# Performance work log

Measured on AMD Instinct MI355X. Metric: run time of the kernel, lower is better.

## Reference

```python
import jax, jax.numpy as jnp
import numpy as np

D_MODEL = 1024
N_HEADS = 16
D_K = D_MODEL // N_HEADS
SEQ = 4096
BATCH = 2
THETA = 10000.0


def _rope(x, token_positions):
    # x: [b, h, s, d_k], token_positions: [s] int
    half = D_K // 2
    inv_freq = 1.0 / (THETA ** (jnp.arange(0, D_K, 2, dtype=jnp.float32) / D_K))  # [half]
    freqs = token_positions.astype(jnp.float32)[:, None] * inv_freq[None, :]      # [s, half]
    cos, sin = jnp.cos(freqs), jnp.sin(freqs)                                     # [s, half]
    xe = x[..., 0::2]
    xo = x[..., 1::2]
    out_e = xe * cos - xo * sin
    out_o = xe * sin + xo * cos
    # interleave even/odd back: [..., s, half, 2] -> [..., s, d_k]
    return jnp.stack([out_e, out_o], axis=-1).reshape(x.shape)


def setup_inputs() -> dict:
    key = jax.random.key(0)
    ks = jax.random.split(key, 5)
    std = (2.0 / (D_MODEL + D_MODEL)) ** 0.5
    x = jax.random.normal(ks[0], (BATCH, SEQ, D_MODEL), dtype=jnp.float32)
    Wq = jax.random.normal(ks[1], (D_MODEL, D_MODEL), dtype=jnp.float32) * std
    Wk = jax.random.normal(ks[2], (D_MODEL, D_MODEL), dtype=jnp.float32) * std
    Wv = jax.random.normal(ks[3], (D_MODEL, D_MODEL), dtype=jnp.float32) * std
    Wo = jax.random.normal(ks[4], (D_MODEL, D_MODEL), dtype=jnp.float32) * std
    token_positions = jnp.arange(SEQ, dtype=jnp.int32)
    return {"x": x, "token_positions": token_positions, "Wq": Wq, "Wk": Wk, "Wv": Wv, "Wo": Wo}


def reference(x, token_positions, Wq, Wk, Wv, Wo):
    B, S, _ = x.shape

    def proj(W):
        y = jnp.einsum('bsd,od->bso', x, W)                     # [b, s, d_model]
        return y.reshape(B, S, N_HEADS, D_K).transpose(0, 2, 1, 3)  # [b, h, s, d_k]

    q, k, v = proj(Wq), proj(Wk), proj(Wv)
    q = _rope(q, token_positions)
    k = _rope(k, token_positions)

    scale = 1.0 / np.sqrt(D_K).astype(np.float32)
    scores = jnp.einsum('bhqd,bhkd->bhqk', q, k) * scale        # [b, h, s, s]
    causal = jnp.tril(jnp.ones((S, S), dtype=bool))
    scores = jnp.where(causal[None, None], scores, -jnp.inf)
    probs = jax.nn.softmax(scores, axis=-1)
    out = jnp.einsum('bhqk,bhkd->bhqd', probs, v)               # [b, h, s, d_k]
    out = out.transpose(0, 2, 1, 3).reshape(B, S, D_MODEL)
    return jnp.einsum('bsd,od->bso', out, Wo)
```

## Files before the change

kernel.cpp:

```cpp
#include <hip/hip_runtime.h>
#include <hip/hip_bf16.h>

typedef unsigned short u16;
typedef __attribute__((ext_vector_type(4))) float f32x4;
typedef __attribute__((ext_vector_type(16))) float f32x16;
typedef __attribute__((ext_vector_type(8))) short s16x8;
typedef __attribute__((ext_vector_type(2))) unsigned u32x2;

constexpr int DMODEL = 1024;
constexpr int NH     = 16;
constexpr int DK     = 64;
constexpr int SEQ    = 4096;
constexpr int BATCH  = 2;
constexpr int BS     = BATCH * SEQ;
constexpr int NX     = BS * DMODEL;
constexpr int NW     = DMODEL * DMODEL;
constexpr float QSC  = 0.18033688011112042f;

__device__ __forceinline__ unsigned pk2(float a, float b) {
  float2 t; t.x = a; t.y = b;
  __hip_bfloat162 h = __float22bfloat162_rn(t);
  return *reinterpret_cast<unsigned*>(&h);
}
__device__ __forceinline__ u32x2 plswap(unsigned a, unsigned b) {
  return __builtin_amdgcn_permlane32_swap(a, b, false, false);
}
__device__ __forceinline__ f32x16 mfma32(s16x8 a, s16x8 b, f32x16 c) {
  return __builtin_amdgcn_mfma_f32_32x32x16_bf16(a, b, c, 0, 0, 0);
}
__device__ __forceinline__ void gload_lds16(const void* g, void* l) {
  __builtin_amdgcn_global_load_lds(
      (const __attribute__((address_space(1))) void*)g,
      (__attribute__((address_space(3))) void*)l, 16, 0, 0);
}
__device__ __forceinline__ float exp2raw(float x) {
  return __builtin_amdgcn_exp2f(x);
}

constexpr int NTCONV = (NX + 4 * NW) / 4 / 256;
__global__ __launch_bounds__(256) void convert_all(
    const float* __restrict__ x, const float* __restrict__ wq,
    const float* __restrict__ wk, const float* __restrict__ wv,
    const float* __restrict__ wo, u16* __restrict__ xb, u16* __restrict__ Wb,
    const int* __restrict__ pos, float2* __restrict__ tab) {
  if (blockIdx.x >= NTCONV) {
    int t = (blockIdx.x - NTCONV) * 256 + threadIdx.x;
    const int s = t >> 5, i = t & 31;
    const float inv = expf(-(float)i * 0.28782313662425574f);
    const float ang = (float)pos[s] * inv;
    float sn, cs;
    sincosf(ang, &sn, &cs);
    tab[t] = make_float2(cs, sn);
    return;
  }
  int t = blockIdx.x * 256 + threadIdx.x;
  int i = t * 4;
  const float* src; u16* dst;
  if (i < NX) { src = x + i; dst = xb + i; }
  else {
    int j = i - NX; int w = j >> 20; int jj = j & (NW - 1);
    src = (w == 0 ? wq : w == 1 ? wk : w == 2 ? wv : wo) + jj;
    dst = Wb + j;
  }
  float4 v = *reinterpret_cast<const float4*>(src);
  uint2 pk; pk.x = pk2(v.x, v.y); pk.y = pk2(v.z, v.w);
  *reinterpret_cast<uint2*>(dst) = pk;
}

__global__ __launch_bounds__(256) void gemm_qkv(
    const u16* __restrict__ A, const u16* __restrict__ Wb,
    u16* __restrict__ Qw, u16* __restrict__ Kw, u16* __restrict__ Vt,
    const float2* __restrict__ tab) {
  __shared__ u16 lA[128 * 32];
  __shared__ u16 lB[128 * 32];
  const int tid = threadIdx.x, w = tid >> 6, l = tid & 63;
  const int wr = w >> 1, wc = w & 1;
  const int id = blockIdx.x;
  const int xcd = id & 7, local = id >> 3;
  const int m_loc = local & 7, n_idx = local >> 3;
  const bool isV = n_idx >= 16;
  const int m0 = (xcd * 8 + m_loc) * 128;
  const int n0 = (isV ? n_idx - 16 : n_idx) * 128;
  const u16* B = Wb + (isV ? 2 * (size_t)NW : 0);
  constexpr int K = 1024;
  f32x4 acc[4][4] = {};
  const int li = l & 15, lg = l >> 4;
  const int srow = l >> 2, skc = (l & 3) * 8;
  for (int k0 = 0; k0 < K; k0 += 32) {
    __syncthreads();
#pragma unroll
    for (int cc = 0; cc < 2; ++cc) {
      const int c = 2 * w + cc;
      const int row = c * 16 + srow;
      gload_lds16(A + (size_t)(m0 + row) * K + k0 + skc, &lA[c * 512]);
      gload_lds16(B + (size_t)(n0 + row) * K + k0 + skc, &lB[c * 512]);
    }
    __syncthreads();
    s16x8 af[4], bfr[4];
#pragma unroll
    for (int i = 0; i < 4; ++i)
      af[i] = *reinterpret_cast<const s16x8*>(&lA[(wr * 64 + i * 16 + li) * 32 + lg * 8]);
#pragma unroll
    for (int j = 0; j < 4; ++j)
      bfr[j] = *reinterpret_cast<const s16x8*>(&lB[(wc * 64 + j * 16 + li) * 32 + lg * 8]);
    if (isV) {
#pragma unroll
      for (int i = 0; i < 4; ++i)
#pragma unroll
        for (int j = 0; j < 4; ++j)
          acc[i][j] = __builtin_amdgcn_mfma_f32_16x16x32_bf16(af[i], bfr[j], acc[i][j], 0, 0, 0);
    } else {
#pragma unroll
      for (int i = 0; i < 4; ++i)
#pragma unroll
        for (int j = 0; j < 4; ++j)
          acc[i][j] = __builtin_amdgcn_mfma_f32_16x16x32_bf16(bfr[j], af[i], acc[i][j], 0, 0, 0);
    }
  }
  if (!isV) {
#pragma unroll
    for (int i = 0; i < 4; ++i) {
#pragma unroll
      for (int j = 0; j < 4; ++j) {
        const int m = m0 + wr * 64 + i * 16 + li;
        const int bb = m >> 12, s = m & (SEQ - 1);
        const int n = n0 + wc * 64 + j * 16 + lg * 4;
        const int which = n >> 10, nn = n & 1023, h = nn >> 6, d0 = nn & 63;
        const int i0 = d0 >> 1;
        const float2 cs0 = tab[s * 32 + i0];
        const float2 cs1 = tab[s * 32 + i0 + 1];
        float oe0 = acc[i][j][0] * cs0.x - acc[i][j][1] * cs0.y;
        float oo0 = acc[i][j][0] * cs0.y + acc[i][j][1] * cs0.x;
        float oe1 = acc[i][j][2] * cs1.x - acc[i][j][3] * cs1.y;
        float oo1 = acc[i][j][2] * cs1.y + acc[i][j][3] * cs1.x;
        if (which == 0) { oe0 *= QSC; oo0 *= QSC; oe1 *= QSC; oo1 *= QSC; }
        u16* dst = (which == 0 ? Qw : Kw) + ((size_t)(bb * NH + h) * SEQ + s) * DK + d0;
        uint2 pk; pk.x = pk2(oe0, oo0); pk.y = pk2(oe1, oo1);
        *reinterpret_cast<uint2*>(dst) = pk;
      }
    }
  } else {
#pragma unroll
    for (int i = 0; i < 4; ++i) {
#pragma unroll
      for (int j = 0; j < 4; ++j) {
        const int mbase = m0 + wr * 64 + i * 16 + lg * 4;
        const int b = mbase >> 12, s0 = mbase & (SEQ - 1);
        const int n = n0 + wc * 64 + j * 16 + li;
        const int h = n >> 6, d = n & 63;
        u16* dst = Vt + ((size_t)(b * NH + h) * DK + d) * SEQ + s0;
        uint2 pk;
        pk.x = pk2(acc[i][j][0], acc[i][j][1]);
        pk.y = pk2(acc[i][j][2], acc[i][j][3]);
        *reinterpret_cast<uint2*>(dst) = pk;
      }
    }
  }
}

__global__ __launch_bounds__(256) void gemm_out(
    const u16* __restrict__ A, const u16* __restrict__ B, float* __restrict__ Co) {
  __shared__ u16 lA[128 * 32];
  __shared__ u16 lB[128 * 32];
  const int tid = threadIdx.x, w = tid >> 6, l = tid & 63;
  const int wr = w >> 1, wc = w & 1;
  const int id = blockIdx.x;
  const int xcd = id & 7, local = id >> 3;
  const int m_loc = local & 7, n_idx = local >> 3;
  const int m0 = (xcd * 8 + m_loc) * 128, n0 = n_idx * 128;
  constexpr int K = 1024;
  f32x4 acc[4][4] = {};
  const int li = l & 15, lg = l >> 4;
  const int srow = l >> 2, skc = (l & 3) * 8;
  for (int k0 = 0; k0 < K; k0 += 32) {
    __syncthreads();
#pragma unroll
    for (int cc = 0; cc < 2; ++cc) {
      const int c = 2 * w + cc;
      const int row = c * 16 + srow;
      gload_lds16(A + (size_t)(m0 + row) * K + k0 + skc, &lA[c * 512]);
      gload_lds16(B + (size_t)(n0 + row) * K + k0 + skc, &lB[c * 512]);
    }
    __syncthreads();
    s16x8 af[4], bfr[4];
#pragma unroll
    for (int i = 0; i < 4; ++i)
      af[i] = *reinterpret_cast<const s16x8*>(&lA[(wr * 64 + i * 16 + li) * 32 + lg * 8]);
#pragma unroll
    for (int j = 0; j < 4; ++j)
      bfr[j] = *reinterpret_cast<const s16x8*>(&lB[(wc * 64 + j * 16 + li) * 32 + lg * 8]);
#pragma unroll
    for (int i = 0; i < 4; ++i)
#pragma unroll
      for (int j = 0; j < 4; ++j)
        acc[i][j] = __builtin_amdgcn_mfma_f32_16x16x32_bf16(bfr[j], af[i], acc[i][j], 0, 0, 0);
  }
#pragma unroll
  for (int i = 0; i < 4; ++i) {
#pragma unroll
    for (int j = 0; j < 4; ++j) {
      const int m = m0 + wr * 64 + i * 16 + li;
      const int n = n0 + wc * 64 + j * 16 + lg * 4;
      float4 v;
      v.x = acc[i][j][0]; v.y = acc[i][j][1]; v.z = acc[i][j][2]; v.w = acc[i][j][3];
      *reinterpret_cast<float4*>(&Co[(size_t)m * DMODEL + n]) = v;
    }
  }
}

__global__ __launch_bounds__(256, 2) void attn_kernel(
    const u16* __restrict__ Qw, const u16* __restrict__ Kw,
    const u16* __restrict__ Vt, u16* __restrict__ Ob) {
  __shared__ __align__(16) u16 Kb[2][8192];
  __shared__ __align__(16) u16 Vb[2][8192];
  const int tid = threadIdx.x, w = tid >> 6, l = tid & 63;
  const int lq = l & 31, hi = l >> 5;
  const int id = blockIdx.x;
  const int g = (id & 7) * 64 + (id >> 3);
  const int bh = g >> 4;
  const int j  = g & 15;
  const int tA = 31 - j, tB = j;
  const int nA = 32 - j;
  const int ntot = 33;
  const u16* Qh = Qw + (size_t)bh * SEQ * DK;
  const u16* Kh = Kw + (size_t)bh * SEQ * DK;
  const u16* Vh = Vt + (size_t)bh * DK * SEQ;
  const int b = bh >> 4, h = bh & 15;

  const s16x8 ones = {(short)0x3F80, (short)0x3F80, (short)0x3F80, (short)0x3F80,
                      (short)0x3F80, (short)0x3F80, (short)0x3F80, (short)0x3F80};

  s16x8 aq[4];
  f32x16 o0, o1, ls;

  auto loadQ = [&](int q0) {
#pragma unroll
    for (int ds = 0; ds < 4; ++ds)
      aq[ds] = *reinterpret_cast<const s16x8*>(
          &Qh[(size_t)(q0 + lq) * DK + ds * 16 + hi * 8]);
  };
  auto resetState = [&]() { o0 = f32x16{}; o1 = f32x16{}; ls = f32x16{}; };
  auto writeO = [&](int q0) {
    const float inv = 1.f / ls[0];
    u16* orow = Ob + ((size_t)(b * SEQ + q0 + lq)) * DMODEL + h * DK;
#pragma unroll
    for (int m = 0; m < 4; ++m) {
      uint2 pa;
      pa.x = pk2(o0[4 * m + 0] * inv, o0[4 * m + 1] * inv);
      pa.y = pk2(o0[4 * m + 2] * inv, o0[4 * m + 3] * inv);
      *reinterpret_cast<uint2*>(orow + 8 * m + 4 * hi) = pa;
      uint2 pb;
      pb.x = pk2(o1[4 * m + 0] * inv, o1[4 * m + 1] * inv);
      pb.y = pk2(o1[4 * m + 2] * inv, o1[4 * m + 3] * inv);
      *reinterpret_cast<uint2*>(orow + 32 + 8 * m + 4 * hi) = pb;
    }
  };
  auto stage = [&](int buf, int kt) {
    const int krow = tid >> 3;
    const int kcol = ((tid & 7) * 16) ^ ((krow & 7) << 4);
#pragma unroll
    for (int i = 0; i < 4; ++i)
      gload_lds16((const char*)Kh + (size_t)(kt + i * 32 + krow) * 128 + kcol,
                  (char*)&Kb[buf][0] + i * 4096 + tid * 16);
    const int vrow = tid >> 4;
    const int vcol = ((tid & 15) * 16) ^ ((vrow & 7) << 4);
#pragma unroll
    for (int i = 0; i < 4; ++i)
      gload_lds16((const char*)Vh + (size_t)(i * 16 + vrow) * (SEQ * 2) + kt * 2 + vcol,
                  (char*)&Vb[buf][0] + i * 4096 + tid * 16);
  };

  int q0 = tA * 128 + w * 32;
  loadQ(q0);
  resetState();
  stage(0, 0);
  int kt = 0;
  for (int it = 0; it < ntot; ++it) {
    asm volatile("s_waitcnt vmcnt(0)" ::: "memory");
    __builtin_amdgcn_s_barrier();
    __builtin_amdgcn_sched_barrier(0);
    const int itn = it + 1;
    const int ktn = (itn < nA) ? 128 * itn : (itn < ntot ? 128 * (itn - nA) : 0);
    stage(itn & 1, ktn);
    const int cur = it & 1;
#pragma unroll
    for (int sub = 0; sub < 2; ++sub) {
      const int ksub = kt + sub * 64;
      if (ksub > q0 + 31) continue;
      f32x16 s0 = {}, s1 = {};
      const char* kb = (const char*)&Kb[cur][0] + (sub * 64 + lq) * 128;
      __builtin_amdgcn_s_setprio(1);
#pragma unroll
      for (int ds = 0; ds < 4; ++ds) {
        const int co = (ds * 32 + hi * 16) ^ ((lq & 7) << 4);
        s16x8 k0 = *reinterpret_cast<const s16x8*>(kb + co);
        s16x8 k1 = *reinterpret_cast<const s16x8*>(kb + 32 * 128 + co);
        s0 = mfma32(k0, aq[ds], s0);
        s1 = mfma32(k1, aq[ds], s1);
      }
      __builtin_amdgcn_s_setprio(0);
      if (ksub + 63 > q0) {
#pragma unroll
        for (int r = 0; r < 16; ++r) {
          const int kr = (r & 3) + 8 * (r >> 2) + 4 * hi;
          if (ksub + kr > q0 + lq) s0[r] = -1e30f;
          if (ksub + 32 + kr > q0 + lq) s1[r] = -1e30f;
        }
      }
#pragma unroll
      for (int r = 0; r < 16; ++r) s0[r] = exp2raw(s0[r]);
#pragma unroll
      for (int r = 0; r < 16; ++r) s1[r] = exp2raw(s1[r]);
      unsigned U0[8], U1[8];
#pragma unroll
      for (int m = 0; m < 4; ++m) {
        U0[m * 2 + 0] = pk2(s0[4 * m + 0], s0[4 * m + 1]);
        U0[m * 2 + 1] = pk2(s0[4 * m + 2], s0[4 * m + 3]);
        U1[m * 2 + 0] = pk2(s1[4 * m + 0], s1[4 * m + 1]);
        U1[m * 2 + 1] = pk2(s1[4 * m + 2], s1[4 * m + 3]);
      }
      const char* vb = (const char*)&Vb[cur][0];
#pragma unroll
      for (int c16 = 0; c16 < 4; ++c16) {
        unsigned* U = (c16 < 2) ? U0 : U1;
        const int m0i = (c16 & 1) * 2, m1i = m0i + 1;
        u32x2 r0 = plswap(U[m0i * 2 + 0], U[m1i * 2 + 0]);
        u32x2 r1 = plswap(U[m0i * 2 + 1], U[m1i * 2 + 1]);
        union { uint4 u; s16x8 s; } cf;
        cf.u.x = r0.x; cf.u.y = r1.x; cf.u.z = r0.y; cf.u.w = r1.y;
        const int co = (sub * 128 + c16 * 32 + hi * 16) ^ ((lq & 7) << 4);
        s16x8 v0 = *reinterpret_cast<const s16x8*>(vb + lq * 256 + co);
        s16x8 v1 = *reinterpret_cast<const s16x8*>(vb + (32 + lq) * 256 + co);
        __builtin_amdgcn_s_setprio(1);
        o0 = mfma32(v0, cf.s, o0);
        o1 = mfma32(v1, cf.s, o1);
        ls = mfma32(ones, cf.s, ls);
        __builtin_amdgcn_s_setprio(0);
      }
    }
    if (it == nA - 1) {
      writeO(q0);
      q0 = tB * 128 + w * 32;
      loadQ(q0);
      resetState();
    }
    kt = ktn;
  }
  writeO(q0);
}

extern "C" void kernel_launch(void* const* d_in, const int* in_sizes, int n_in,
                              void* d_out, int out_size, void* d_ws, size_t ws_size,
                              hipStream_t stream) {
  const float* x  = (const float*)d_in[0];
  const int*  pos = (const int*)d_in[1];
  const float* wq = (const float*)d_in[2];
  const float* wk = (const float*)d_in[3];
  const float* wv = (const float*)d_in[4];
  const float* wo = (const float*)d_in[5];
  float* out = (float*)d_out;

  u16* Wb = (u16*)d_ws;
  u16* xb = Wb + 4 * (size_t)NW;
  u16* Qw = xb + (size_t)NX;
  u16* Kw = Qw + (size_t)NX;
  u16* Vt = Kw + (size_t)NX;
  float2* tab = (float2*)(Vt + (size_t)NX);
  u16* Ab = xb;

  convert_all<<<NTCONV + 512, 256, 0, stream>>>(x, wq, wk, wv, wo, xb, Wb, pos, tab);
  gemm_qkv<<<1536, 256, 0, stream>>>(xb, Wb, Qw, Kw, Vt, tab);
  attn_kernel<<<512, 256, 0, stream>>>(Qw, Kw, Vt, Ab);
  gemm_out<<<512, 256, 0, stream>>>(Ab, Wb + 3 * (size_t)NW, out);
}
```

Measured before the change: 226.5 us.

## Process two 32-row query subtiles per wave and compute row sums via VALU

Each wave now owns 64 query rows (two 32-row subtiles) in a 256-row block tile, reusing each K/V LDS fragment for both subtiles. This replaces the paired-tile (tA/tB) causal balancing with a per-XCD ordering in which bh and tile index are chosen from the block id. The ones-matrix MFMA that produced the softmax denominator is replaced by a VALU sum plus a permlane swap. It doubles accumulator registers, which may hurt occupancy under launch_bounds(256,2), and the workload per block is now uneven, ranging from 2 to 32 iterations.

```diff
diff --git a/kernel.cpp b/kernel.cpp
--- a/kernel.cpp
+++ b/kernel.cpp
@@ -22,6 +22,8 @@
   __hip_bfloat162 h = __float22bfloat162_rn(t);
   return *reinterpret_cast<unsigned*>(&h);
 }
+__device__ __forceinline__ unsigned fbits(float f) { union { float f; unsigned u; } v; v.f = f; return v.u; }
+__device__ __forceinline__ float bitsf(unsigned u) { union { unsigned u; float f; } v; v.u = u; return v.f; }
 __device__ __forceinline__ u32x2 plswap(unsigned a, unsigned b) {
   return __builtin_amdgcn_permlane32_swap(a, b, false, false);
 }
@@ -216,33 +218,84 @@
   const int tid = threadIdx.x, w = tid >> 6, l = tid & 63;
   const int lq = l & 31, hi = l >> 5;
   const int id = blockIdx.x;
-  const int g = (id & 7) * 64 + (id >> 3);
-  const int bh = g >> 4;
-  const int j  = g & 15;
-  const int tA = 31 - j, tB = j;
-  const int nA = 32 - j;
-  const int ntot = 33;
+  const int xcd = id & 7, local = id >> 3;
+  const int seg = local >> 4, within = local & 15;
+  const int t = (seg < 2) ? (15 - within) : within;
+  const int bh = xcd * 4 + seg;
+  const int niter = 2 * (t + 1);
   const u16* Qh = Qw + (size_t)bh * SEQ * DK;
   const u16* Kh = Kw + (size_t)bh * SEQ * DK;
   const u16* Vh = Vt + (size_t)bh * DK * SEQ;
   const int b = bh >> 4, h = bh & 15;
-
-  const s16x8 ones = {(short)0x3F80, (short)0x3F80, (short)0x3F80, (short)0x3F80,
-                      (short)0x3F80, (short)0x3F80, (short)0x3F80, (short)0x3F80};
-
-  s16x8 aq[4];
-  f32x16 o0, o1, ls;
-
-  auto loadQ = [&](int q0) {
-#pragma unroll
-    for (int ds = 0; ds < 4; ++ds)
-      aq[ds] = *reinterpret_cast<const s16x8*>(
-          &Qh[(size_t)(q0 + lq) * DK + ds * 16 + hi * 8]);
+  const int q0 = t * 256 + w * 64;
+
+  s16x8 aqA[4], aqB[4];
+#pragma unroll
+  for (int ds = 0; ds < 4; ++ds) {
+    aqA[ds] = *reinterpret_cast<const s16x8*>(
+        &Qh[(size_t)(q0 + lq) * DK + ds * 16 + hi * 8]);
+    aqB[ds] = *reinterpret_cast<const s16x8*>(
+        &Qh[(size_t)(q0 + 32 + lq) * DK + ds * 16 + hi * 8]);
+  }
+  f32x16 oA0 = {}, oA1 = {}, oB0 = {}, oB1 = {};
+  float lsA = 0.f, lsB = 0.f;
+
+  auto stage = [&](int buf, int kt) {
+    const int krow = tid >> 3;
+    const int kcol = ((tid & 7) * 16) ^ ((krow & 7) << 4);
+#pragma unroll
+    for (int i = 0; i < 4; ++i)
+      gload_lds16((const char*)Kh + (size_t)(kt + i * 32 + krow) * 128 + kcol,
+                  (char*)&Kb[buf][0] + i * 4096 + tid * 16);
+    const int vrow = tid >> 4;
+    const int vcol = ((tid & 15) * 16) ^ ((vrow & 7) << 4);
+#pragma unroll
+    for (int i = 0; i < 4; ++i)
+      gload_lds16((const char*)Vh + (size_t)(i * 16 + vrow) * (SEQ * 2) + kt * 2 + vcol,
+                  (char*)&Vb[buf][0] + i * 4096 + tid * 16);
   };
-  auto resetState = [&]() { o0 = f32x16{}; o1 = f32x16{}; ls = f32x16{}; };
-  auto writeO = [&](int q0) {
-    const float inv = 1.f / ls[0];
-    u16* orow = Ob + ((size_t)(b * SEQ + q0 + lq)) * DMODEL + h * DK;
+  auto smax = [&](f32x16& s0, f32x16& s1, const int qq, const int ksub,
+                  float& lsr, s16x8* p) {
+    if (ksub + 63 > qq) {
+#pragma unroll
+      for (int r = 0; r < 16; ++r) {
+        const int kr = (r & 3) + 8 * (r >> 2) + 4 * hi;
+        if (ksub + kr > qq + lq) s0[r] = -1e30f;
+        if (ksub + 32 + kr > qq + lq) s1[r] = -1e30f;
+      }
+    }
+    float rs = 0.f;
+#pragma unroll
+    for (int r = 0; r < 16; ++r) { s0[r] = exp2raw(s0[r]); rs += s0[r]; }
+#pragma unroll
+    for (int r = 0; r < 16; ++r) { s1[r] = exp2raw(s1[r]); rs += s1[r]; }
+    {
+      u32x2 pr = plswap(fbits(rs), fbits(rs));
+      rs = bitsf(pr.x) + bitsf(pr.y);
+    }
+    lsr += rs;
+    unsigned U0[8], U1[8];
+#pragma unroll
+    for (int m = 0; m < 4; ++m) {
+      U0[m * 2 + 0] = pk2(s0[4 * m + 0], s0[4 * m + 1]);
+      U0[m * 2 + 1] = pk2(s0[4 * m + 2], s0[4 * m + 3]);
+      U1[m * 2 + 0] = pk2(s1[4 * m + 0], s1[4 * m + 1]);
+      U1[m * 2 + 1] = pk2(s1[4 * m + 2], s1[4 * m + 3]);
+    }
+#pragma unroll
+    for (int c16 = 0; c16 < 4; ++c16) {
+      unsigned* U = (c16 < 2) ? U0 : U1;
+      const int m0i = (c16 & 1) * 2, m1i = m0i + 1;
+      u32x2 r0 = plswap(U[m0i * 2 + 0], U[m1i * 2 + 0]);
+      u32x2 r1 = plswap(U[m0i * 2 + 1], U[m1i * 2 + 1]);
+      union { uint4 u; s16x8 s; } cf;
+      cf.u.x = r0.x; cf.u.y = r1.x; cf.u.z = r0.y; cf.u.w = r1.y;
+      p[c16] = cf.s;
+    }
+  };
+  auto writeO = [&](int qs, const f32x16& o0, const f32x16& o1, float lsr) {
+    const float inv = 1.f / lsr;
+    u16* orow = Ob + ((size_t)(b * SEQ + qs + lq)) * DMODEL + h * DK;
 #pragma unroll
     for (int m = 0; m < 4; ++m) {
       uint2 pa;
@@ -255,98 +308,74 @@
       *reinterpret_cast<uint2*>(orow + 32 + 8 * m + 4 * hi) = pb;
     }
   };
-  auto stage = [&](int buf, int kt) {
-    const int krow = tid >> 3;
-    const int kcol = ((tid & 7) * 16) ^ ((krow & 7) << 4);
-#pragma unroll
-    for (int i = 0; i < 4; ++i)
-      gload_lds16((const char*)Kh + (size_t)(kt + i * 32 + krow) * 128 + kcol,
-                  (char*)&Kb[buf][0] + i * 4096 + tid * 16);
-    const int vrow = tid >> 4;
-    const int vcol = ((tid & 15) * 16) ^ ((vrow & 7) << 4);
-#pragma unroll
-    for (int i = 0; i < 4; ++i)
-      gload_lds16((const char*)Vh + (size_t)(i * 16 + vrow) * (SEQ * 2) + kt * 2 + vcol,
-                  (char*)&Vb[buf][0] + i * 4096 + tid * 16);
-  };
-
-  int q0 = tA * 128 + w * 32;
-  loadQ(q0);
-  resetState();
+
   stage(0, 0);
   int kt = 0;
-  for (int it = 0; it < ntot; ++it) {
+  for (int it = 0; it < niter; ++it) {
     asm volatile("s_waitcnt vmcnt(0)" ::: "memory");
     __builtin_amdgcn_s_barrier();
     __builtin_amdgcn_sched_barrier(0);
     const int itn = it + 1;
-    const int ktn = (itn < nA) ? 128 * itn : (itn < ntot ? 128 * (itn - nA) : 0);
+    const int ktn = (itn < niter) ? 128 * itn : 0;
     stage(itn & 1, ktn);
     const int cur = it & 1;
 #pragma unroll
     for (int sub = 0; sub < 2; ++sub) {
       const int ksub = kt + sub * 64;
-      if (ksub > q0 + 31) continue;
-      f32x16 s0 = {}, s1 = {};
-      const char* kb = (const char*)&Kb[cur][0] + (sub * 64 + lq) * 128;
-      __builtin_amdgcn_s_setprio(1);
+      if (ksub > q0 + 63) continue;
+      const bool do0 = (ksub <= q0 + 31);
+      const int sw = (lq & 7) << 4;
+      s16x8 kf0[4], kf1[4];
+      const char* kb = (const char*)&Kb[cur][0] + (size_t)(sub * 64 + lq) * 128;
 #pragma unroll
       for (int ds = 0; ds < 4; ++ds) {
-        const int co = (ds * 32 + hi * 16) ^ ((lq & 7) << 4);
-        s16x8 k0 = *reinterpret_cast<const s16x8*>(kb + co);
-        s16x8 k1 = *reinterpret_cast<const s16x8*>(kb + 32 * 128 + co);
-        s0 = mfma32(k0, aq[ds], s0);
-        s1 = mfma32(k1, aq[ds], s1);
-      }
-      __builtin_amdgcn_s_setprio(0);
-      if (ksub + 63 > q0) {
-#pragma unroll
-        for (int r = 0; r < 16; ++r) {
-          const int kr = (r & 3) + 8 * (r >> 2) + 4 * hi;
-          if (ksub + kr > q0 + lq) s0[r] = -1e30f;
-          if (ksub + 32 + kr > q0 + lq) s1[r] = -1e30f;
+        const int co = (ds * 32 + hi * 16) ^ sw;
+        kf0[ds] = *reinterpret_cast<const s16x8*>(kb + co);
+        kf1[ds] = *reinterpret_cast<const s16x8*>(kb + 32 * 128 + co);
+      }
+      s16x8 p0[4], p1[4];
+      {
+        f32x16 s0 = {}, s1 = {};
+        __builtin_amdgcn_s_setprio(1);
+#pragma unroll
+        for (int ds = 0; ds < 4; ++ds) {
+          s0 = mfma32(kf0[ds], aqB[ds], s0);
+          s1 = mfma32(kf1[ds], aqB[ds], s1);
         }
-      }
-#pragma unroll
-      for (int r = 0; r < 16; ++r) s0[r] = exp2raw(s0[r]);
-#pragma unroll
-      for (int r = 0; r < 16; ++r) s1[r] = exp2raw(s1[r]);
-      unsigned U0[8], U1[8];
-#pragma unroll
-      for (int m = 0; m < 4; ++m) {
-        U0[m * 2 + 0] = pk2(s0[4 * m + 0], s0[4 * m + 1]);
-        U0[m * 2 + 1] = pk2(s0[4 * m + 2], s0[4 * m + 3]);
-        U1[m * 2 + 0] = pk2(s1[4 * m + 0], s1[4 * m + 1]);
-        U1[m * 2 + 1] = pk2(s1[4 * m + 2], s1[4 * m + 3]);
+        __builtin_amdgcn_s_setprio(0);
+        smax(s0, s1, q0 + 32, ksub, lsB, p1);
+      }
+      if (do0) {
+        f32x16 s0 = {}, s1 = {};
+        __builtin_amdgcn_s_setprio(1);
+#pragma unroll
+        for (int ds = 0; ds < 4; ++ds) {
+          s0 = mfma32(kf0[ds], aqA[ds], s0);
+          s1 = mfma32(kf1[ds], aqA[ds], s1);
+        }
+        __builtin_amdgcn_s_setprio(0);
+        smax(s0, s1, q0, ksub, lsA, p0);
       }
       const char* vb = (const char*)&Vb[cur][0];
 #pragma unroll
       for (int c16 = 0; c16 < 4; ++c16) {
-        unsigned* U = (c16 < 2) ? U0 : U1;
-        const int m0i = (c16 & 1) * 2, m1i = m0i + 1;
-        u32x2 r0 = plswap(U[m0i * 2 + 0], U[m1i * 2 + 0]);
-        u32x2 r1 = plswap(U[m0i * 2 + 1], U[m1i * 2 + 1]);
-        union { uint4 u; s16x8 s; } cf;
-        cf.u.x = r0.x; cf.u.y = r1.x; cf.u.z = r0.y; cf.u.w = r1.y;
-        const int co = (sub * 128 + c16 * 32 + hi * 16) ^ ((lq & 7) << 4);
-        s16x8 v0 = *reinterpret_cast<const s16x8*>(vb + lq * 256 + co);
-        s16x8 v1 = *reinterpret_cast<const s16x8*>(vb + (32 + lq) * 256 + co);
+        const int co = (sub * 128 + c16 * 32 + hi * 16) ^ sw;
+        s16x8 v0 = *reinterpret_cast<const s16x8*>(vb + (size_t)lq * 256 + co);
+        s16x8 v1 = *reinterpret_cast<const s16x8*>(vb + (size_t)(32 + lq) * 256 + co);
         __builtin_amdgcn_s_setprio(1);
-        o0 = mfma32(v0, cf.s, o0);
-        o1 = mfma32(v1, cf.s, o1);
-        ls = mfma32(ones, cf.s, ls);
+        if (do0) {
+          oA0 = mfma32(v0, p0[c16], oA0);
+          oA1 = mfma32(v1, p0[c16], oA1);
+        }
+        oB0 = mfma32(v0, p1[c16], oB0);
+        oB1 = mfma32(v1, p1[c16], oB1);
         __builtin_amdgcn_s_setprio(0);
       }
     }
-    if (it == nA - 1) {
-      writeO(q0);
-      q0 = tB * 128 + w * 32;
-      loadQ(q0);
-      resetState();
-    }
     kt = ktn;
   }
-  writeO(q0);
+  writeO(q0, oA0, oA1, lsA);
+  writeO(q0 + 32, oB0, oB1, lsB);
 }
 
 extern "C" void kernel_launch(void* const* d_in, const int* in_sizes, int n_in,
```

Measured after the change: 240.0 us. +6.0%, slower.
